# Performance work log

Hardware: AMD Instinct MI355X
Metric: run time of the kernel (lower is better)

Reference implementation:

```python
import jax, jax.numpy as jnp
import numpy as np


def setup_inputs() -> dict:
    key = jax.random.key(0)
    B, T = 4096, 2048
    # small positive strains keep C = 2E + I symmetric positive definite
    strain = jax.random.uniform(key, (B, T, 3), dtype=jnp.float32) * 0.2
    ki0 = jnp.float32(1.5)  # learned exponent for order-0 stretch term
    ki1 = jnp.float32(1.0)  # scale on log(J) term (init 1.0 in torch code)
    return {"strain": strain, "ki0": ki0, "ki1": ki1}


def reference(strain, ki0, ki1):
    # Build symmetric 2x2 right Cauchy-Green tensor C = 2E + I implicitly:
    # E00 = s0, E11 = s1, E01 = E10 = 0.5*s2  ->  C01 = s2
    c00 = 2.0 * strain[..., 0] + 1.0          # [B, T]
    c11 = 2.0 * strain[..., 1] + 1.0
    c01 = strain[..., 2]

    det = c00 * c11 - c01 * c01               # det(C)
    J = jnp.sqrt(det)
    log_J = jnp.log(J)

    # closed-form eigenvalues of symmetric 2x2, ascending (matches eigvalsh)
    mean = 0.5 * (c00 + c11)
    rad = jnp.sqrt(0.25 * (c00 - c11) ** 2 + c01 * c01)
    sq_eig = jnp.stack([mean - rad, mean + rad], axis=-1)  # [B, T, 2]

    eig = jnp.sqrt(sq_eig)                    # principal stretches
    aux = J ** (-1.0 / 3.0)                   # volumetric regularizer
    reg_eig = eig * aux[..., None]            # [B, T, 2]

    # order_stretches = 1: one powered-stretch block + scaled log(J)
    kan_input = jnp.concatenate(
        [reg_eig ** ki0, (log_J * ki1)[..., None]], axis=-1
    )                                         # [B, T, 3]
    return kan_input
```

## Files before the change

kernel.cpp:

```cpp
#include <hip/hip_runtime.h>


typedef unsigned int u32;

__device__ __forceinline__ void compute3(float s0, float s1, float s2,
                                         float ki0, float ki1,
                                         float& o0, float& o1, float& o2) {
    const float c00 = __builtin_fmaf(2.0f, s0, 1.0f);
    const float c11 = __builtin_fmaf(2.0f, s1, 1.0f);
    const float c01 = s2;
    const float det = c00 * c11 - c01 * c01;
    const float l2det = __builtin_log2f(det);
    const float mean = 0.5f * (c00 + c11);
    const float diff = 0.5f * (c00 - c11);
    const float rad  = __builtin_sqrtf(__builtin_fmaf(diff, diff, c01 * c01));
    const float l2a = -0.16666666667f * l2det;
    o0 = __builtin_exp2f(ki0 * __builtin_fmaf(0.5f, __builtin_log2f(mean - rad), l2a));
    o1 = __builtin_exp2f(ki0 * __builtin_fmaf(0.5f, __builtin_log2f(mean + rad), l2a));
    o2 = (0.34657359028f * l2det) * ki1;
}

constexpr int TPB       = 256;
constexpr int TRIPT     = 8;
constexpr int TILE_TRIP = TPB * TRIPT;
constexpr int CHT       = 6;
constexpr int TILE_CH   = TPB * CHT;
constexpr int ROW_SLOTS = 7;

__global__ __launch_bounds__(TPB) void kan_v6_lds(
    const float* __restrict__ strain,
    const float* __restrict__ ki0p,
    const float* __restrict__ ki1p,
    float* __restrict__ out,
    long long ntrip)
{
    __shared__ float4 lds4[TPB * ROW_SLOTS];

    const float ki0 = ki0p[0];
    const float ki1 = ki1p[0];
    const int t = threadIdx.x;
    const long long full_tiles = ntrip / TILE_TRIP;

    for (long long tile = blockIdx.x; tile < full_tiles; tile += gridDim.x) {
        const long long cbase = tile * TILE_CH;
        const float4* in4 = (const float4*)strain + cbase;
        float4*      out4 = (float4*)out + cbase;

        __syncthreads();
#pragma unroll
        for (int j = 0; j < CHT; ++j) {
            const u32 k = (u32)t + (u32)(j * TPB);
            lds4[(k / 6u) * ROW_SLOTS + (k % 6u)] = in4[k];
        }
        __syncthreads();

        const int rb = t * ROW_SLOTS;
        const float4 r0 = lds4[rb + 0], r1 = lds4[rb + 1], r2 = lds4[rb + 2];
        const float4 r3 = lds4[rb + 3], r4 = lds4[rb + 4], r5 = lds4[rb + 5];

        float o[24];
        compute3(r0.x, r0.y, r0.z, ki0, ki1, o[0],  o[1],  o[2]);
        compute3(r0.w, r1.x, r1.y, ki0, ki1, o[3],  o[4],  o[5]);
        compute3(r1.z, r1.w, r2.x, ki0, ki1, o[6],  o[7],  o[8]);
        compute3(r2.y, r2.z, r2.w, ki0, ki1, o[9],  o[10], o[11]);
        compute3(r3.x, r3.y, r3.z, ki0, ki1, o[12], o[13], o[14]);
        compute3(r3.w, r4.x, r4.y, ki0, ki1, o[15], o[16], o[17]);
        compute3(r4.z, r4.w, r5.x, ki0, ki1, o[18], o[19], o[20]);
        compute3(r5.y, r5.z, r5.w, ki0, ki1, o[21], o[22], o[23]);

        __syncthreads();
        lds4[rb + 0] = make_float4(o[0],  o[1],  o[2],  o[3]);
        lds4[rb + 1] = make_float4(o[4],  o[5],  o[6],  o[7]);
        lds4[rb + 2] = make_float4(o[8],  o[9],  o[10], o[11]);
        lds4[rb + 3] = make_float4(o[12], o[13], o[14], o[15]);
        lds4[rb + 4] = make_float4(o[16], o[17], o[18], o[19]);
        lds4[rb + 5] = make_float4(o[20], o[21], o[22], o[23]);
        __syncthreads();

#pragma unroll
        for (int j = 0; j < CHT; ++j) {
            const u32 k = (u32)t + (u32)(j * TPB);
            out4[k] = lds4[(k / 6u) * ROW_SLOTS + (k % 6u)];
        }
    }

    const long long tail_start = full_tiles * TILE_TRIP;
    const long long gs = (long long)gridDim.x * TPB;
    for (long long e = tail_start + (long long)blockIdx.x * TPB + t; e < ntrip; e += gs) {
        float o0, o1, o2;
        compute3(strain[3 * e], strain[3 * e + 1], strain[3 * e + 2],
                 ki0, ki1, o0, o1, o2);
        out[3 * e]     = o0;
        out[3 * e + 1] = o1;
        out[3 * e + 2] = o2;
    }
}

extern "C" void kernel_launch(void* const* d_in, const int* in_sizes, int n_in,
                              void* d_out, int out_size, void* d_ws, size_t ws_size,
                              hipStream_t stream) {
    const float* strain = (const float*)d_in[0];
    const float* ki0p   = (const float*)d_in[1];
    const float* ki1p   = (const float*)d_in[2];
    float* out = (float*)d_out;

    const long long ntrip = (long long)in_sizes[0] / 3;
    long long blocks = ntrip / TILE_TRIP;
    if (blocks < 1) blocks = 1;
    if (blocks > 32768) blocks = 32768;

    kan_v6_lds<<<(int)blocks, TPB, 0, stream>>>(strain, ki0p, ki1p, out, ntrip);
}
```

Baseline: 182.5 us.

## Replace LDS transpose with wavefront shuffles to realign float4 triplets

Removes the shared-memory staging tile and its four barriers. Each thread now loads one float4 directly and rebuilds the 3-float triplets that cross float4 boundaries with neighbour lane shuffles. Wave-edge lanes fall back to extra global loads. Each thread evaluates two compute3 calls per float4, so the transcendental work rises by about half. The grid becomes a grid-stride loop capped at 4096 blocks, each handling 512 float4s per iteration.

```diff
diff --git a/kernel.cpp b/kernel.cpp
--- a/kernel.cpp
+++ b/kernel.cpp
@@ -20,73 +20,88 @@
     o2 = (0.34657359028f * l2det) * ki1;
 }
 
-constexpr int TPB       = 256;
-constexpr int TRIPT     = 8;
-constexpr int TILE_TRIP = TPB * TRIPT;
-constexpr int CHT       = 6;
-constexpr int TILE_CH   = TPB * CHT;
-constexpr int ROW_SLOTS = 7;
+__device__ __forceinline__ float4 process4(float4 v, u32 g, int l, u32 nf4,
+                                           float ki0, float ki1,
+                                           const float* __restrict__ gf) {
+    const u32 r = g % 3u;
+    float pw = __shfl_up(v.w, 1);
+    float nx = __shfl_down(v.x, 1);
 
-__global__ __launch_bounds__(TPB) void kan_v6_lds(
+    const bool last  = (l == 63) || (g == nf4 - 1u);
+    const bool first = (l == 0);
+    float e0 = 0.0f, e1 = 0.0f;
+    if (last) {
+        if (r == 1u)      nx = gf[(size_t)4 * g + 4];
+        else if (r == 0u) { e0 = gf[(size_t)4 * g + 4]; e1 = gf[(size_t)4 * g + 5]; }
+    }
+    if (first) {
+        if (r == 1u)      pw = gf[(size_t)4 * g - 1];
+        else if (r == 2u) { e0 = gf[(size_t)4 * g - 2]; e1 = gf[(size_t)4 * g - 1]; }
+    }
+    const bool fixN = last  && (r == 0u);
+    const bool fixP = first && (r == 2u);
+
+    const float pa = (r == 0u) ? v.x : (r == 1u) ? pw  : v.y;
+    const float pb = (r == 0u) ? v.y : (r == 1u) ? v.x : v.z;
+    const float pc = (r == 0u) ? v.z : (r == 1u) ? v.y : v.w;
+    const float sa = fixN ? v.w : fixP ? e0  : v.z;
+    const float sb = fixN ? e0  : fixP ? e1  : v.w;
+    const float sc = fixN ? e1  : fixP ? v.x : nx;
+
+    float Po0, Po1, Po2, So0, So1, So2;
+    compute3(pa, pb, pc, ki0, ki1, Po0, Po1, Po2);
+    compute3(sa, sb, sc, ki0, ki1, So0, So1, So2);
+
+    const float nPo0 = __shfl_down(Po0, 1);
+    const float pSo2 = __shfl_up(So2, 1);
+
+    float4 o;
+    if (r == 0u) {
+        o.x = Po0; o.y = Po1; o.z = Po2; o.w = last ? So0 : nPo0;
+    } else if (r == 1u) {
+        o.x = Po1; o.y = Po2; o.z = So0; o.w = So1;
+    } else {
+        o.x = fixP ? So2 : pSo2; o.y = Po0; o.z = Po1; o.w = Po2;
+    }
+    return o;
+}
+
+constexpr int TPB = 256;
+
+__global__ __launch_bounds__(TPB) void kan_v7_shfl(
     const float* __restrict__ strain,
     const float* __restrict__ ki0p,
     const float* __restrict__ ki1p,
     float* __restrict__ out,
-    long long ntrip)
+    int nfloat_i)
 {
-    __shared__ float4 lds4[TPB * ROW_SLOTS];
-
     const float ki0 = ki0p[0];
     const float ki1 = ki1p[0];
-    const int t = threadIdx.x;
-    const long long full_tiles = ntrip / TILE_TRIP;
+    const u32 nfloat = (u32)nfloat_i;
+    const u32 nf4 = nfloat >> 2;
+    const u32 t = threadIdx.x;
+    const int l = (int)(t & 63u);
+    const float4* __restrict__ in4  = (const float4*)strain;
+    float4* __restrict__ out4 = (float4*)out;
 
-    for (long long tile = blockIdx.x; tile < full_tiles; tile += gridDim.x) {
-        const long long cbase = tile * TILE_CH;
-        const float4* in4 = (const float4*)strain + cbase;
-        float4*      out4 = (float4*)out + cbase;
-
-        __syncthreads();
-#pragma unroll
-        for (int j = 0; j < CHT; ++j) {
-            const u32 k = (u32)t + (u32)(j * TPB);
-            lds4[(k / 6u) * ROW_SLOTS + (k % 6u)] = in4[k];
-        }
-        __syncthreads();
-
-        const int rb = t * ROW_SLOTS;
-        const float4 r0 = lds4[rb + 0], r1 = lds4[rb + 1], r2 = lds4[rb + 2];
-        const float4 r3 = lds4[rb + 3], r4 = lds4[rb + 4], r5 = lds4[rb + 5];
-
-        float o[24];
-        compute3(r0.x, r0.y, r0.z, ki0, ki1, o[0],  o[1],  o[2]);
-        compute3(r0.w, r1.x, r1.y, ki0, ki1, o[3],  o[4],  o[5]);
-        compute3(r1.z, r1.w, r2.x, ki0, ki1, o[6],  o[7],  o[8]);
-        compute3(r2.y, r2.z, r2.w, ki0, ki1, o[9],  o[10], o[11]);
-        compute3(r3.x, r3.y, r3.z, ki0, ki1, o[12], o[13], o[14]);
-        compute3(r3.w, r4.x, r4.y, ki0, ki1, o[15], o[16], o[17]);
-        compute3(r4.z, r4.w, r5.x, ki0, ki1, o[18], o[19], o[20]);
-        compute3(r5.y, r5.z, r5.w, ki0, ki1, o[21], o[22], o[23]);
-
-        __syncthreads();
-        lds4[rb + 0] = make_float4(o[0],  o[1],  o[2],  o[3]);
-        lds4[rb + 1] = make_float4(o[4],  o[5],  o[6],  o[7]);
-        lds4[rb + 2] = make_float4(o[8],  o[9],  o[10], o[11]);
-        lds4[rb + 3] = make_float4(o[12], o[13], o[14], o[15]);
-        lds4[rb + 4] = make_float4(o[16], o[17], o[18], o[19]);
-        lds4[rb + 5] = make_float4(o[20], o[21], o[22], o[23]);
-        __syncthreads();
-
-#pragma unroll
-        for (int j = 0; j < CHT; ++j) {
-            const u32 k = (u32)t + (u32)(j * TPB);
-            out4[k] = lds4[(k / 6u) * ROW_SLOTS + (k % 6u)];
-        }
+    const u32 chunk = 2u * (u32)TPB;
+    const u32 step = gridDim.x * chunk;
+    for (u32 base = blockIdx.x * chunk; base < nf4; base += step) {
+        const u32 g0 = base + t;
+        const u32 g1 = base + (u32)TPB + t;
+        const bool h0 = g0 < nf4;
+        const bool h1 = g1 < nf4;
+        float4 v0, v1;
+        if (h0) v0 = in4[g0];
+        if (h1) v1 = in4[g1];
+        if (h0) out4[g0] = process4(v0, g0, l, nf4, ki0, ki1, strain);
+        if (h1) out4[g1] = process4(v1, g1, l, nf4, ki0, ki1, strain);
     }
 
-    const long long tail_start = full_tiles * TILE_TRIP;
-    const long long gs = (long long)gridDim.x * TPB;
-    for (long long e = tail_start + (long long)blockIdx.x * TPB + t; e < ntrip; e += gs) {
+    const u32 ntrip = nfloat / 3u;
+    const u32 t0 = (nf4 * 4u) / 3u;
+    const u32 gs = gridDim.x * (u32)TPB;
+    for (u32 e = t0 + blockIdx.x * (u32)TPB + t; e < ntrip; e += gs) {
         float o0, o1, o2;
         compute3(strain[3 * e], strain[3 * e + 1], strain[3 * e + 2],
                  ki0, ki1, o0, o1, o2);
@@ -104,10 +119,11 @@
     const float* ki1p   = (const float*)d_in[2];
     float* out = (float*)d_out;
 
-    const long long ntrip = (long long)in_sizes[0] / 3;
-    long long blocks = ntrip / TILE_TRIP;
-    if (blocks < 1) blocks = 1;
-    if (blocks > 32768) blocks = 32768;
+    const int nfloat = in_sizes[0];
+    const u32 nf4 = ((u32)nfloat) >> 2;
+    u32 blocks = (nf4 + 511u) / 512u;
+    if (blocks > 4096u) blocks = 4096u;
+    if (blocks < 1u) blocks = 1u;
 
-    kan_v6_lds<<<(int)blocks, TPB, 0, stream>>>(strain, ki0p, ki1p, out, ntrip);
+    kan_v7_shfl<<<(int)blocks, TPB, 0, stream>>>(strain, ki0p, ki1p, out, nfloat);
 }
```

After: 180.0 us. About the same (-1.4%).
